# Kernel tuning notes

Hardware: AMD Instinct MI355X
Metric: run time of the kernel (lower is better)

The kernel has to match this reference:

```python
import jax, jax.numpy as jnp
import numpy as np

N_NODES = 50000


def _gcn_norm(edge_index, num_nodes):
    # add self loops, compute symmetric normalization D^-1/2 (A+I) D^-1/2
    loops = jnp.arange(num_nodes, dtype=edge_index.dtype)
    row = jnp.concatenate([edge_index[0], loops])
    col = jnp.concatenate([edge_index[1], loops])
    deg = jax.ops.segment_sum(jnp.ones_like(row, dtype=jnp.float32), col,
                              num_segments=num_nodes)
    dinv = jnp.where(deg > 0, jax.lax.rsqrt(deg), 0.0)
    norm = dinv[row] * dinv[col]  # [E']
    return row, col, norm


def _gcn_conv(x, W, b, row, col, norm, num_nodes):
    h = x @ W                       # [N, out] transform first (smaller dim)
    msg = h[row] * norm[:, None]    # gather along source nodes  [E', out]
    agg = jax.ops.segment_sum(msg, col, num_segments=num_nodes)  # scatter-add
    return agg + b


def setup_inputs() -> dict:
    key = jax.random.key(0)
    k1, k2, k3, k4 = jax.random.split(key, 4)
    x = jax.random.normal(k1, (N_NODES, 128), dtype=jnp.float32)
    edge_index = jax.random.randint(k2, (2, 800000), 0, N_NODES, dtype=jnp.int64)
    W1 = jax.random.normal(k3, (128, 128), dtype=jnp.float32) * (1.0 / np.sqrt(128))
    b1 = jnp.zeros((128,), dtype=jnp.float32)
    W2 = jax.random.normal(k4, (128, 16), dtype=jnp.float32) * (1.0 / np.sqrt(128))
    b2 = jnp.zeros((16,), dtype=jnp.float32)
    return {"x": x, "edge_index": edge_index, "W1": W1, "b1": b1, "W2": W2, "b2": b2}


def reference(x, edge_index, W1, b1, W2, b2):
    n = x.shape[0]
    row, col, norm = _gcn_norm(edge_index, n)
    h = _gcn_conv(x, W1, b1, row, col, norm, n)
    h = jax.nn.relu(h)
    h = _gcn_conv(h, W2, b2, row, col, norm, n)
    return jax.nn.log_softmax(h, axis=1)
```

## Files before the change

kernel.cpp:

```cpp
#include <hip/hip_runtime.h>
#include <math.h>

constexpr int N  = 50000;
constexpr int E  = 800000;
constexpr int F1 = 128;
constexpr int F2 = 16;
constexpr int BSHIFT  = 8;
constexpr int NBUCKET = (N + 255) >> BSHIFT;
constexpr int CHUNK   = 2048;
constexpr int CAP     = 6144;
constexpr int SBLK    = (E + CHUNK - 1) / CHUNK;
constexpr int GBLK    = 391;
constexpr int CSTRIDE = 32;

typedef unsigned short ushort_t;
typedef unsigned char  uchar_t;
typedef __bf16 bf16x8 __attribute__((ext_vector_type(8)));
typedef float  f32x4  __attribute__((ext_vector_type(4)));

static __device__ __forceinline__ float blo(unsigned u) { return __uint_as_float(u << 16); }
static __device__ __forceinline__ float bhi(unsigned u) { return __uint_as_float(u & 0xffff0000u); }
static __device__ __forceinline__ ushort_t to_bf(float f) { __bf16 h = (__bf16)f; return *(ushort_t*)&h; }
static __device__ __forceinline__ uchar_t to_fp8(float f) {
    return (uchar_t)(__builtin_amdgcn_cvt_pk_fp8_f32(f, f, 0, false) & 0xff);
}
template <int S>
static __device__ __forceinline__ float cf8(unsigned u) {
    return __builtin_amdgcn_cvt_f32_fp8(u, S);
}

__global__ __launch_bounds__(256) void k_scatterP_gemm1(const int* __restrict__ row,
                                                        const int* __restrict__ col,
                                                        int* __restrict__ cursor,
                                                        unsigned* __restrict__ P,
                                                        const float* __restrict__ x,
                                                        const float* __restrict__ W1,
                                                        uchar_t* __restrict__ h1q) {
    __shared__ ushort_t Wl[F1 * 136];
    int t = threadIdx.x;

    if (blockIdx.x < SBLK) {
        int* hist = (int*)Wl;
        int* cur  = hist + NBUCKET;
        if (t < NBUCKET) hist[t] = 0;
        __syncthreads();
        int base = blockIdx.x * CHUNK;
        int ce[CHUNK / 256];
#pragma unroll
        for (int i = 0; i < CHUNK / 256; ++i) {
            int e = base + i * 256 + t;
            ce[i] = (e < E) ? col[e] : -1;
            if (ce[i] >= 0) atomicAdd(&hist[ce[i] >> BSHIFT], 1);
        }
        __syncthreads();
        if (t < NBUCKET) cur[t] = t * CAP + atomicAdd(&cursor[t * CSTRIDE], hist[t]);
        __syncthreads();
#pragma unroll
        for (int i = 0; i < CHUNK / 256; ++i) {
            int e = base + i * 256 + t;
            if (ce[i] >= 0) {
                int c = ce[i];
                int pos = atomicAdd(&cur[c >> BSHIFT], 1);
                P[pos] = ((unsigned)row[e] << BSHIFT) | (unsigned)(c & 255);
            }
        }
        return;
    }

    int gb = blockIdx.x - SBLK;
    {
        int n = t & 127, kh = t >> 7;
#pragma unroll
        for (int j = 0; j < 8; ++j) {
            int k0 = (kh * 8 + j) * 8;
            bf16x8 w;
#pragma unroll
            for (int i2 = 0; i2 < 8; ++i2) w[i2] = (__bf16)W1[(k0 + i2) * F1 + n];
            *(bf16x8*)&Wl[n * 136 + k0] = w;
        }
    }
    __syncthreads();

    int lane = t & 63, wv = t >> 6;
    int quad = lane >> 4, l15 = lane & 15;
#pragma unroll 1
    for (int tile = gb * 2; tile < gb * 2 + 2; ++tile) {
        int arow = tile * 64 + wv * 16 + l15;
        int rclamp = min(arow, N - 1);
        f32x4 acc[8] = {};
#pragma unroll
        for (int kk = 0; kk < 4; ++kk) {
            int k0 = kk * 32 + quad * 8;
            const float* xp = x + (size_t)rclamp * F1 + k0;
            float4 u0 = *(const float4*)xp;
            float4 u1 = *(const float4*)(xp + 4);
            bf16x8 a;
            a[0] = (__bf16)u0.x; a[1] = (__bf16)u0.y; a[2] = (__bf16)u0.z; a[3] = (__bf16)u0.w;
            a[4] = (__bf16)u1.x; a[5] = (__bf16)u1.y; a[6] = (__bf16)u1.z; a[7] = (__bf16)u1.w;
#pragma unroll
            for (int ct = 0; ct < 8; ++ct) {
                bf16x8 b = *(const bf16x8*)&Wl[(ct * 16 + l15) * 136 + k0];
                acc[ct] = __builtin_amdgcn_mfma_f32_16x16x32_bf16(a, b, acc[ct], 0, 0, 0);
            }
        }
        int orow0 = tile * 64 + wv * 16 + quad * 4;
#pragma unroll
        for (int r = 0; r < 4; ++r) {
            int orow = orow0 + r;
            if (orow < N) {
#pragma unroll
                for (int ct = 0; ct < 8; ++ct)
                    h1q[(size_t)orow * F1 + ct * 16 + l15] = to_fp8(acc[ct][r]);
            }
        }
    }
}

__global__ __launch_bounds__(512) void k_binFinal(const unsigned* __restrict__ P,
                                                  const int* __restrict__ cursor,
                                                  ushort_t* __restrict__ csr16,
                                                  int* __restrict__ seg_start,
                                                  int* __restrict__ counts,
                                                  float* __restrict__ dinv) {
    __shared__ unsigned eb[CAP];
    __shared__ int cnt[256];
    __shared__ int cur[256];
    __shared__ int wtot[4];
    int t = threadIdx.x;
    int b = blockIdx.x;
    int lo = b << BSHIFT;
    int n_nodes = min(256, N - lo);
    int m = cursor[b * CSTRIDE];
    if (t < 256) cnt[t] = 0;
    __syncthreads();
    const unsigned* Pb = P + (size_t)b * CAP;
    for (int k = t; k < m; k += 512) {
        unsigned u = Pb[k];
        eb[k] = u;
        atomicAdd(&cnt[u & 255], 1);
    }
    __syncthreads();
    int lane = t & 63, wid = t >> 6;
    int v = 0, incl = 0;
    if (t < 256) {
        v = cnt[t];
        incl = v;
#pragma unroll
        for (int d = 1; d < 64; d <<= 1) {
            int u = __shfl_up(incl, d, 64);
            if (lane >= d) incl += u;
        }
        if (lane == 63) wtot[wid] = incl;
    }
    __syncthreads();
    if (t < 256) {
        int wb = 0;
        for (int w = 0; w < wid; ++w) wb += wtot[w];
        int o = b * CAP + wb + incl - v;
        cur[t] = o;
        if (t < n_nodes) {
            seg_start[lo + t] = o;
            counts[lo + t] = v;
            dinv[lo + t] = rsqrtf((float)v + 1.f);
        }
    }
    __syncthreads();
    for (int k = t; k < m; k += 512) {
        unsigned u = eb[k];
        int pos = atomicAdd(&cur[u & 255], 1);
        csr16[pos] = (ushort_t)(u >> BSHIFT);
    }
}

__global__ __launch_bounds__(256) void k_gather1_gemm2(const uchar_t* __restrict__ h1q,
                                                       const int* __restrict__ seg_start,
                                                       const int* __restrict__ counts,
                                                       const ushort_t* __restrict__ csr16,
                                                       const float* __restrict__ dinv,
                                                       const float* __restrict__ W2,
                                                       const float* __restrict__ b1,
                                                       ushort_t* __restrict__ h2s) {
    __shared__ __align__(16) ushort_t W2l[F2 * 136];
    __shared__ __align__(16) ushort_t T[16 * 136];
    __shared__ float dv[16];
    int t = threadIdx.x;
    for (int i = t; i < F1 * F2; i += 256) {
        int k = i >> 4, n = i & 15;
        W2l[n * 136 + k] = to_bf(W2[i]);
    }
    int lane = t & 63, wv = t >> 6;
    int g = lane >> 4, l15 = lane & 15;
    int gbase = lane & 48;
    int nl = wv * 4 + g;
    int c = blockIdx.x * 16 + nl;
    int cl = min(c, N - 1);

    float dc = 0.f;
    int s = seg_start[cl];
    int cnt = 0;
    if (c < N) { dc = dinv[c]; cnt = counts[c]; }
    int mcnt = cnt;
    mcnt = max(mcnt, __shfl_xor(mcnt, 16));
    mcnt = max(mcnt, __shfl_xor(mcnt, 32));

    float a0 = 0.f, a1 = 0.f, a2 = 0.f, a3 = 0.f;
    float a4 = 0.f, a5 = 0.f, a6 = 0.f, a7 = 0.f;

#define G1FLT(j_, jb_) { unsigned u = __shfl(pk, gbase + (jb_) + (j_));                     \
        e##j_ = __uint_as_float(u & 0xffff0000u);                                           \
        w##j_ = *(const uint2*)(h1q + ((size_t)(u & 0xffffu) << 7) + (l15 << 3)); }
#define G1ACC(j_) {                                                                         \
        a0 = fmaf(e##j_, cf8<0>(w##j_.x), a0); a1 = fmaf(e##j_, cf8<1>(w##j_.x), a1);       \
        a2 = fmaf(e##j_, cf8<2>(w##j_.x), a2); a3 = fmaf(e##j_, cf8<3>(w##j_.x), a3);       \
        a4 = fmaf(e##j_, cf8<0>(w##j_.y), a4); a5 = fmaf(e##j_, cf8<1>(w##j_.y), a5);       \
        a6 = fmaf(e##j_, cf8<2>(w##j_.y), a6); a7 = fmaf(e##j_, cf8<3>(w##j_.y), a7); }

#pragma unroll 1
    for (int k0 = 0; k0 < mcnt; k0 += 16) {
        unsigned pk = 0;
        int k = k0 + l15;
        if (k < cnt) {
            int r = csr16[s + k];
            pk = ((unsigned)to_bf(dinv[r]) << 16) | (unsigned)r;
        }
        {
            uint2 w0, w1, w2, w3, w4, w5, w6, w7;
            float e0, e1, e2, e3, e4, e5, e6, e7;
            G1FLT(0, 0) G1FLT(1, 0) G1FLT(2, 0) G1FLT(3, 0)
            G1FLT(4, 0) G1FLT(5, 0) G1FLT(6, 0) G1FLT(7, 0)
            G1ACC(0) G1ACC(1) G1ACC(2) G1ACC(3)
            G1ACC(4) G1ACC(5) G1ACC(6) G1ACC(7)
        }
        if (k0 + 8 < mcnt) {
            uint2 w0, w1, w2, w3, w4, w5, w6, w7;
            float e0, e1, e2, e3, e4, e5, e6, e7;
            G1FLT(0, 8) G1FLT(1, 8) G1FLT(2, 8) G1FLT(3, 8)
            G1FLT(4, 8) G1FLT(5, 8) G1FLT(6, 8) G1FLT(7, 8)
            G1ACC(0) G1ACC(1) G1ACC(2) G1ACC(3)
            G1ACC(4) G1ACC(5) G1ACC(6) G1ACC(7)
        }
    }
#undef G1FLT
#undef G1ACC

    {
        uint2 ws = *(const uint2*)(h1q + ((size_t)cl << 7) + (l15 << 3));
        a0 = fmaf(dc, cf8<0>(ws.x), a0); a1 = fmaf(dc, cf8<1>(ws.x), a1);
        a2 = fmaf(dc, cf8<2>(ws.x), a2); a3 = fmaf(dc, cf8<3>(ws.x), a3);
        a4 = fmaf(dc, cf8<0>(ws.y), a4); a5 = fmaf(dc, cf8<1>(ws.y), a5);
        a6 = fmaf(dc, cf8<2>(ws.y), a6); a7 = fmaf(dc, cf8<3>(ws.y), a7);
        float4 bL = ((const float4*)b1)[l15 * 2];
        float4 bH = ((const float4*)b1)[l15 * 2 + 1];
        a0 = fmaxf(fmaf(dc, a0, bL.x), 0.f); a1 = fmaxf(fmaf(dc, a1, bL.y), 0.f);
        a2 = fmaxf(fmaf(dc, a2, bL.z), 0.f); a3 = fmaxf(fmaf(dc, a3, bL.w), 0.f);
        a4 = fmaxf(fmaf(dc, a4, bH.x), 0.f); a5 = fmaxf(fmaf(dc, a5, bH.y), 0.f);
        a6 = fmaxf(fmaf(dc, a6, bH.z), 0.f); a7 = fmaxf(fmaf(dc, a7, bH.w), 0.f);
        uint4 pp;
        pp.x = (unsigned)to_bf(a0) | ((unsigned)to_bf(a1) << 16);
        pp.y = (unsigned)to_bf(a2) | ((unsigned)to_bf(a3) << 16);
        pp.z = (unsigned)to_bf(a4) | ((unsigned)to_bf(a5) << 16);
        pp.w = (unsigned)to_bf(a6) | ((unsigned)to_bf(a7) << 16);
        *(uint4*)&T[nl * 136 + (l15 << 3)] = pp;
        if (l15 == 0) dv[nl] = dc;
    }
    __syncthreads();

    if (wv == 0) {
        int quad = lane >> 4;
        f32x4 acc = {};
#pragma unroll
        for (int kk = 0; kk < 4; ++kk) {
            int k0 = kk * 32 + quad * 8;
            bf16x8 a = *(const bf16x8*)&T[l15 * 136 + k0];
            bf16x8 b = *(const bf16x8*)&W2l[l15 * 136 + k0];
            acc = __builtin_amdgcn_mfma_f32_16x16x32_bf16(a, b, acc, 0, 0, 0);
        }
#pragma unroll
        for (int r = 0; r < 4; ++r) {
            int rw = quad * 4 + r;
            int gn = blockIdx.x * 16 + rw;
            if (gn < N) h2s[(size_t)gn * F2 + l15] = to_bf(acc[r] * dv[rw]);
        }
    }
}

__global__ __launch_bounds__(256) void k_gather2(const ushort_t* __restrict__ h2s,
                                                 const int* __restrict__ seg_start,
                                                 const int* __restrict__ counts,
                                                 const ushort_t* __restrict__ csr16,
                                                 const float* __restrict__ dinv,
                                                 const float* __restrict__ b2,
                                                 float* __restrict__ out) {
    int idx = blockIdx.x * 256 + threadIdx.x;
    int node = idx >> 3, sub = idx & 7;
    if (node >= N) return;
    int lane = threadIdx.x & 63;
    int gb = lane & 56;
    int s = seg_start[node], cntc = counts[node];
    float ax = 0.f, ay = 0.f;

#define G2LOAD(n_) { int src = gb | min(n_, rem - 1); int r = __shfl(rl, src);              \
        w##n_ = ((const unsigned*)(h2s + (size_t)r * F2))[sub]; if (n_ >= rem) w##n_ = 0u; }

#pragma unroll 1
    for (int j0 = 0; j0 < cntc; j0 += 8) {
        int rem = min(cntc - j0, 8);
        int rl = 0;
        if (sub < rem) rl = csr16[s + j0 + sub];
        unsigned w0, w1, w2, w3, w4, w5, w6, w7;
        G2LOAD(0) G2LOAD(1) G2LOAD(2) G2LOAD(3)
        G2LOAD(4) G2LOAD(5) G2LOAD(6) G2LOAD(7)
        ax += ((blo(w0) + blo(w1)) + (blo(w2) + blo(w3))) +
              ((blo(w4) + blo(w5)) + (blo(w6) + blo(w7)));
        ay += ((bhi(w0) + bhi(w1)) + (bhi(w2) + bhi(w3))) +
              ((bhi(w4) + bhi(w5)) + (bhi(w6) + bhi(w7)));
    }
#undef G2LOAD
    unsigned us = ((const unsigned*)(h2s + (size_t)node * F2))[sub];
    ax += blo(us);
    ay += bhi(us);
    float dc = dinv[node];
    float2 bb = ((const float2*)b2)[sub];
    float v0 = fmaf(dc, ax, bb.x);
    float v1 = fmaf(dc, ay, bb.y);
    float mx = fmaxf(v0, v1);
#pragma unroll
    for (int m = 1; m < 8; m <<= 1) mx = fmaxf(mx, __shfl_xor(mx, m));
    float sm = expf(v0 - mx) + expf(v1 - mx);
#pragma unroll
    for (int m = 1; m < 8; m <<= 1) sm += __shfl_xor(sm, m);
    float lse = mx + logf(sm);
    float2 o;
    o.x = v0 - lse;
    o.y = v1 - lse;
    ((float2*)(out + (size_t)node * F2))[sub] = o;
}

extern "C" void kernel_launch(void* const* d_in, const int* in_sizes, int n_in,
                              void* d_out, int out_size, void* d_ws, size_t ws_size,
                              hipStream_t stream) {
    const float* x  = (const float*)d_in[0];
    const int*   ei = (const int*)d_in[1];
    const float* W1 = (const float*)d_in[2];
    const float* b1 = (const float*)d_in[3];
    const float* W2 = (const float*)d_in[4];
    const float* b2 = (const float*)d_in[5];
    const int* row = ei;
    const int* col = ei + E;

    char* ws = (char*)d_ws;
    int*      cursor    = (int*)ws;      ws += 256 * CSTRIDE * 4;
    unsigned* P         = (unsigned*)ws; ws += (size_t)NBUCKET * CAP * 4;
    ushort_t* csr16     = (ushort_t*)ws; ws += (size_t)NBUCKET * CAP * 2;
    int*      seg_start = (int*)ws;      ws += (size_t)N * 4;
    int*      counts    = (int*)ws;      ws += (size_t)N * 4;
    float*    dinv      = (float*)ws;    ws += (size_t)N * 4;
    uchar_t*  h1q       = (uchar_t*)ws;  ws += (size_t)N * F1;
    ushort_t* h2s       = (ushort_t*)ws; ws += (size_t)N * F2 * 2;

    (void)hipMemsetAsync(cursor, 0, 256 * CSTRIDE * 4, stream);

    k_scatterP_gemm1<<<SBLK + GBLK, 256, 0, stream>>>(row, col, cursor, P, x, W1, h1q);
    k_binFinal<<<NBUCKET, 512, 0, stream>>>(P, cursor, csr16, seg_start, counts, dinv);
    k_gather1_gemm2<<<(N + 15) / 16, 256, 0, stream>>>(h1q, seg_start, counts, csr16,
                                                       dinv, W2, b1, h2s);
    k_gather2<<<((size_t)N * 8 + 255) / 256, 256, 0, stream>>>(h2s, seg_start, counts, csr16,
                                                               dinv, b2, (float*)d_out);
}
```

Before: 142.9 us.

## Stage bucket scatter in LDS, widen binFinal, prefetch CSR indices in gathers

The scatter phase now sorts each chunk's edges by bucket in shared memory using a block prefix scan, then writes them to global P in contiguous runs instead of scattering each edge with its own atomic-derived address. binFinal is launched with 1024 threads per block instead of 512. Both gather kernels software-pipeline the next batch of CSR indices (and dinv) one iteration ahead and hoist the self-loop, bias and dinv loads to the top of the kernel. These changes aim to hide index-load latency and to coalesce the P writes, at the cost of more LDS use and more registers.

```diff
diff --git a/kernel.cpp b/kernel.cpp
--- a/kernel.cpp
+++ b/kernel.cpp
@@ -36,15 +36,21 @@
                                                         const float* __restrict__ x,
                                                         const float* __restrict__ W1,
                                                         uchar_t* __restrict__ h1q) {
-    __shared__ ushort_t Wl[F1 * 136];
+    __shared__ __align__(16) ushort_t Wl[F1 * 136];
     int t = threadIdx.x;
 
     if (blockIdx.x < SBLK) {
         int* hist = (int*)Wl;
-        int* cur  = hist + NBUCKET;
-        if (t < NBUCKET) hist[t] = 0;
+        int* loff = hist + 256;
+        int* gst  = loff + 256;
+        int* lcur = gst + 256;
+        int* wtot = lcur + 256;
+        unsigned* eb  = (unsigned*)(wtot + 8);
+        uchar_t*  bbk = (uchar_t*)(eb + 2048);
+        int base = blockIdx.x * CHUNK;
+        int total = min(CHUNK, E - base);
+        hist[t] = 0;
         __syncthreads();
-        int base = blockIdx.x * CHUNK;
         int ce[CHUNK / 256];
 #pragma unroll
         for (int i = 0; i < CHUNK / 256; ++i) {
@@ -53,15 +59,42 @@
             if (ce[i] >= 0) atomicAdd(&hist[ce[i] >> BSHIFT], 1);
         }
         __syncthreads();
-        if (t < NBUCKET) cur[t] = t * CAP + atomicAdd(&cursor[t * CSTRIDE], hist[t]);
+        {
+            int lane = t & 63, wid = t >> 6;
+            int v = hist[t];
+            int incl = v;
+#pragma unroll
+            for (int d = 1; d < 64; d <<= 1) {
+                int u = __shfl_up(incl, d, 64);
+                if (lane >= d) incl += u;
+            }
+            if (lane == 63) wtot[wid] = incl;
+            __syncthreads();
+            int wb = 0;
+            for (int w = 0; w < wid; ++w) wb += wtot[w];
+            int ex = wb + incl - v;
+            loff[t] = ex;
+            lcur[t] = ex;
+            if (t < NBUCKET) gst[t] = t * CAP + atomicAdd(&cursor[t * CSTRIDE], v);
+        }
         __syncthreads();
 #pragma unroll
         for (int i = 0; i < CHUNK / 256; ++i) {
             int e = base + i * 256 + t;
             if (ce[i] >= 0) {
-                int c = ce[i];
-                int pos = atomicAdd(&cur[c >> BSHIFT], 1);
-                P[pos] = ((unsigned)row[e] << BSHIFT) | (unsigned)(c & 255);
+                int b = ce[i] >> BSHIFT;
+                int pos = atomicAdd(&lcur[b], 1);
+                eb[pos]  = ((unsigned)row[e] << BSHIFT) | (unsigned)(ce[i] & 255);
+                bbk[pos] = (uchar_t)b;
+            }
+        }
+        __syncthreads();
+#pragma unroll
+        for (int i = 0; i < CHUNK / 256; ++i) {
+            int k = i * 256 + t;
+            if (k < total) {
+                int b = bbk[k];
+                P[gst[b] + (k - loff[b])] = eb[k];
             }
         }
         return;
@@ -116,12 +149,12 @@
     }
 }
 
-__global__ __launch_bounds__(512) void k_binFinal(const unsigned* __restrict__ P,
-                                                  const int* __restrict__ cursor,
-                                                  ushort_t* __restrict__ csr16,
-                                                  int* __restrict__ seg_start,
-                                                  int* __restrict__ counts,
-                                                  float* __restrict__ dinv) {
+__global__ __launch_bounds__(1024) void k_binFinal(const unsigned* __restrict__ P,
+                                                   const int* __restrict__ cursor,
+                                                   ushort_t* __restrict__ csr16,
+                                                   int* __restrict__ seg_start,
+                                                   int* __restrict__ counts,
+                                                   float* __restrict__ dinv) {
     __shared__ unsigned eb[CAP];
     __shared__ int cnt[256];
     __shared__ int cur[256];
@@ -134,7 +167,7 @@
     if (t < 256) cnt[t] = 0;
     __syncthreads();
     const unsigned* Pb = P + (size_t)b * CAP;
-    for (int k = t; k < m; k += 512) {
+    for (int k = t; k < m; k += 1024) {
         unsigned u = Pb[k];
         eb[k] = u;
         atomicAdd(&cnt[u & 255], 1);
@@ -165,7 +198,7 @@
         }
     }
     __syncthreads();
-    for (int k = t; k < m; k += 512) {
+    for (int k = t; k < m; k += 1024) {
         unsigned u = eb[k];
         int pos = atomicAdd(&cur[u & 255], 1);
         csr16[pos] = (ushort_t)(u >> BSHIFT);
@@ -199,6 +232,9 @@
     int s = seg_start[cl];
     int cnt = 0;
     if (c < N) { dc = dinv[c]; cnt = counts[c]; }
+    uint2 wsf = *(const uint2*)(h1q + ((size_t)cl << 7) + (l15 << 3));
+    float4 bL = ((const float4*)b1)[l15 * 2];
+    float4 bH = ((const float4*)b1)[l15 * 2 + 1];
     int mcnt = cnt;
     mcnt = max(mcnt, __shfl_xor(mcnt, 16));
     mcnt = max(mcnt, __shfl_xor(mcnt, 32));
@@ -215,13 +251,21 @@
         a4 = fmaf(e##j_, cf8<0>(w##j_.y), a4); a5 = fmaf(e##j_, cf8<1>(w##j_.y), a5);       \
         a6 = fmaf(e##j_, cf8<2>(w##j_.y), a6); a7 = fmaf(e##j_, cf8<3>(w##j_.y), a7); }
 
-#pragma unroll 1
-    for (int k0 = 0; k0 < mcnt; k0 += 16) {
-        unsigned pk = 0;
-        int k = k0 + l15;
+    unsigned pk = 0;
+    {   int k = l15;
         if (k < cnt) {
             int r = csr16[s + k];
             pk = ((unsigned)to_bf(dinv[r]) << 16) | (unsigned)r;
+        }
+    }
+#pragma unroll 1
+    for (int k0 = 0; k0 < mcnt; k0 += 16) {
+        unsigned pknext = 0;
+        {   int k = k0 + 16 + l15;
+            if (k < cnt) {
+                int r = csr16[s + k];
+                pknext = ((unsigned)to_bf(dinv[r]) << 16) | (unsigned)r;
+            }
         }
         {
             uint2 w0, w1, w2, w3, w4, w5, w6, w7;
@@ -239,18 +283,16 @@
             G1ACC(0) G1ACC(1) G1ACC(2) G1ACC(3)
             G1ACC(4) G1ACC(5) G1ACC(6) G1ACC(7)
         }
+        pk = pknext;
     }
 #undef G1FLT
 #undef G1ACC
 
     {
-        uint2 ws = *(const uint2*)(h1q + ((size_t)cl << 7) + (l15 << 3));
-        a0 = fmaf(dc, cf8<0>(ws.x), a0); a1 = fmaf(dc, cf8<1>(ws.x), a1);
-        a2 = fmaf(dc, cf8<2>(ws.x), a2); a3 = fmaf(dc, cf8<3>(ws.x), a3);
-        a4 = fmaf(dc, cf8<0>(ws.y), a4); a5 = fmaf(dc, cf8<1>(ws.y), a5);
-        a6 = fmaf(dc, cf8<2>(ws.y), a6); a7 = fmaf(dc, cf8<3>(ws.y), a7);
-        float4 bL = ((const float4*)b1)[l15 * 2];
-        float4 bH = ((const float4*)b1)[l15 * 2 + 1];
+        a0 = fmaf(dc, cf8<0>(wsf.x), a0); a1 = fmaf(dc, cf8<1>(wsf.x), a1);
+        a2 = fmaf(dc, cf8<2>(wsf.x), a2); a3 = fmaf(dc, cf8<3>(wsf.x), a3);
+        a4 = fmaf(dc, cf8<0>(wsf.y), a4); a5 = fmaf(dc, cf8<1>(wsf.y), a5);
+        a6 = fmaf(dc, cf8<2>(wsf.y), a6); a7 = fmaf(dc, cf8<3>(wsf.y), a7);
         a0 = fmaxf(fmaf(dc, a0, bL.x), 0.f); a1 = fmaxf(fmaf(dc, a1, bL.y), 0.f);
         a2 = fmaxf(fmaf(dc, a2, bL.z), 0.f); a3 = fmaxf(fmaf(dc, a3, bL.w), 0.f);
         a4 = fmaxf(fmaf(dc, a4, bH.x), 0.f); a5 = fmaxf(fmaf(dc, a5, bH.y), 0.f);
@@ -297,16 +339,22 @@
     int lane = threadIdx.x & 63;
     int gb = lane & 56;
     int s = seg_start[node], cntc = counts[node];
+    float dc = dinv[node];
+    float2 bb = ((const float2*)b2)[sub];
+    unsigned us = ((const unsigned*)(h2s + (size_t)node * F2))[sub];
     float ax = 0.f, ay = 0.f;
 
 #define G2LOAD(n_) { int src = gb | min(n_, rem - 1); int r = __shfl(rl, src);              \
         w##n_ = ((const unsigned*)(h2s + (size_t)r * F2))[sub]; if (n_ >= rem) w##n_ = 0u; }
 
+    int rl = 0;
+    if (sub < min(cntc, 8)) rl = csr16[s + sub];
 #pragma unroll 1
     for (int j0 = 0; j0 < cntc; j0 += 8) {
         int rem = min(cntc - j0, 8);
-        int rl = 0;
-        if (sub < rem) rl = csr16[s + j0 + sub];
+        int rlnext = 0;
+        int j2 = j0 + 8;
+        if (j2 < cntc && sub < cntc - j2) rlnext = csr16[s + j2 + sub];
         unsigned w0, w1, w2, w3, w4, w5, w6, w7;
         G2LOAD(0) G2LOAD(1) G2LOAD(2) G2LOAD(3)
         G2LOAD(4) G2LOAD(5) G2LOAD(6) G2LOAD(7)
@@ -314,13 +362,11 @@
               ((blo(w4) + blo(w5)) + (blo(w6) + blo(w7)));
         ay += ((bhi(w0) + bhi(w1)) + (bhi(w2) + bhi(w3))) +
               ((bhi(w4) + bhi(w5)) + (bhi(w6) + bhi(w7)));
+        rl = rlnext;
     }
 #undef G2LOAD
-    unsigned us = ((const unsigned*)(h2s + (size_t)node * F2))[sub];
     ax += blo(us);
     ay += bhi(us);
-    float dc = dinv[node];
-    float2 bb = ((const float2*)b2)[sub];
     float v0 = fmaf(dc, ax, bb.x);
     float v1 = fmaf(dc, ay, bb.y);
     float mx = fmaxf(v0, v1);
@@ -361,7 +407,7 @@
     (void)hipMemsetAsync(cursor, 0, 256 * CSTRIDE * 4, stream);
 
     k_scatterP_gemm1<<<SBLK + GBLK, 256, 0, stream>>>(row, col, cursor, P, x, W1, h1q);
-    k_binFinal<<<NBUCKET, 512, 0, stream>>>(P, cursor, csr16, seg_start, counts, dinv);
+    k_binFinal<<<NBUCKET, 1024, 0, stream>>>(P, cursor, csr16, seg_start, counts, dinv);
     k_gather1_gemm2<<<(N + 15) / 16, 256, 0, stream>>>(h1q, seg_start, counts, csr16,
                                                        dinv, W2, b1, h2s);
     k_gather2<<<((size_t)N * 8 + 255) / 256, 256, 0, stream>>>(h2s, seg_start, counts, csr16,
```

Result: no change. 142.7 us (-0.1%).
